# Kernel tuning notes

Measured on AMD Instinct MI355X. Metric: run time of the kernel, lower is better.

## Reference

```python
import jax, jax.numpy as jnp
import numpy as np
from jax import lax

H, W = 128, 128
K_JUNC = 300
STEPS = 32
THRESH = 0.008
BIAS_SPAN = 1
SCALE = 5.0
SENTINEL = K_JUNC * K_JUNC


def decode_hafm(angs, dist, bias):
    # angs [B,3,H,W], dist [B,1,H,W], bias [B,1,H,W] -> lines [B,3,H,W,4]
    bias_range = jnp.arange(-BIAS_SPAN, BIAS_SPAN + 1, dtype=jnp.float32).reshape(1, -1, 1, 1)
    d = jnp.clip(dist + bias * bias_range, 0.0, 1.0)  # [B,3,H,W]
    angle0 = (angs[:, 0:1] - 0.5) * jnp.pi * 2
    angle1 = angs[:, 1:2] * jnp.pi / 2
    angle2 = -angs[:, 2:3] * jnp.pi / 2
    c0, s0 = jnp.cos(angle0), jnp.sin(angle0)
    t1, t2 = jnp.tan(angle1), jnp.tan(angle2)
    x1 = (c0 - s0 * t1) * d * SCALE
    y1 = (s0 + c0 * t1) * d * SCALE
    x2 = (c0 - s0 * t2) * d * SCALE
    y2 = (s0 + c0 * t2) * d * SCALE
    y0, x0 = jnp.meshgrid(jnp.arange(H, dtype=jnp.float32), jnp.arange(W, dtype=jnp.float32), indexing='ij')
    x0 = x0[None, None]
    y0 = y0[None, None]
    x1 = jnp.clip(x1 + x0, 0, W - 1)
    y1 = jnp.clip(y1 + y0, 0, H - 1)
    x2 = jnp.clip(x2 + x0, 0, W - 1)
    y2 = jnp.clip(y2 + y0, 0, H - 1)
    return jnp.stack((x1, y1, x2, y2), axis=-1)


def propose_junctions(jloc, joff):
    # jloc [H,W], joff [2,H,W]; 3x3 NMS + top-K, thresholded junctions
    pooled = lax.reduce_window(jloc, -jnp.inf, lax.max, (3, 3), (1, 1), 'SAME')
    nms = jnp.where(jloc == pooled, jloc, 0.0)
    scores, idx = lax.top_k(nms.reshape(-1), K_JUNC)
    y = (idx // W).astype(jnp.float32)
    x = (idx % W).astype(jnp.float32)
    xs = x + joff[0].reshape(-1)[idx]
    ys = y + joff[1].reshape(-1)[idx]
    coords = jnp.stack([xs, ys], axis=-1)  # [K,2]
    valid = scores > THRESH
    coords = jnp.where(valid[:, None], coords, 1e6)
    return coords, scores


def bilinear_sample(fmap, px, py):
    # fmap [C,H,W]; px,py [N,S] -> [C,N,S]
    C = fmap.shape[0]
    px = jnp.clip(px, 0.0, W - 1)
    py = jnp.clip(py, 0.0, H - 1)
    x0 = jnp.floor(px)
    y0 = jnp.floor(py)
    x0i = x0.astype(jnp.int32)
    y0i = y0.astype(jnp.int32)
    x1i = jnp.minimum(x0i + 1, W - 1)
    y1i = jnp.minimum(y0i + 1, H - 1)
    wx = px - x0
    wy = py - y0
    flat = fmap.reshape(C, H * W)

    def g(yi, xi):
        return flat[:, (yi * W + xi).reshape(-1)].reshape(C, *px.shape)

    return (g(y0i, x0i) * (1 - wx) * (1 - wy)
            + g(y0i, x1i) * wx * (1 - wy)
            + g(y1i, x0i) * (1 - wx) * wy
            + g(y1i, x1i) * wx * wy)


def setup_inputs() -> dict:
    key = jax.random.key(0)
    ks = jax.random.split(key, 10)
    return {
        'features': jax.random.normal(ks[0], (1, 256, H, W), jnp.float32),
        'heatmaps': jax.random.normal(ks[1], (1, 9, H, W), jnp.float32),
        'fc1_w': jax.random.normal(ks[2], (128, 256), jnp.float32) * 0.05,
        'fc1_b': jax.random.normal(ks[3], (128,), jnp.float32) * 0.05,
        'w1': jax.random.normal(ks[4], (1024, 1024), jnp.float32) * 0.03,
        'b1': jnp.zeros((1024,), jnp.float32),
        'w2': jax.random.normal(ks[5], (1024, 1024), jnp.float32) * 0.03,
        'b2': jnp.zeros((1024,), jnp.float32),
        'w3': jax.random.normal(ks[6], (1, 1024), jnp.float32) * 0.03,
        'b3': jnp.zeros((1,), jnp.float32),
    }


def reference(features, heatmaps, fc1_w, fc1_b, w1, b1, w2, b2, w3, b3):
    angs = jax.nn.sigmoid(heatmaps[:, 0:3])
    dist = jax.nn.sigmoid(heatmaps[:, 3:4])
    bias = jax.nn.sigmoid(heatmaps[:, 4:5])
    jloc = jax.nn.softmax(heatmaps[:, 5:7], axis=1)[0, 1]  # [H,W]
    joff = jax.nn.sigmoid(heatmaps[0, 7:9])                # [2,H,W]

    junc, _ = propose_junctions(jloc, joff)                # [K,2]
    lines = decode_hafm(angs, dist, bias).reshape(-1, 4)   # [N,4], N=3*H*W
    N = lines.shape[0]

    # junction-to-endpoint matching (cdist + argmin)
    d1 = ((junc[:, None, :] - lines[None, :, :2]) ** 2).sum(-1)  # [K,N]
    d2 = ((junc[:, None, :] - lines[None, :, 2:]) ** 2).sum(-1)
    j1 = jnp.argmin(d1, axis=0)
    j2 = jnp.argmin(d2, axis=0)
    lo = jnp.minimum(j1, j2)
    hi = jnp.maximum(j1, j2)
    ids = jnp.where(lo < hi, lo * K_JUNC + hi, SENTINEL)
    # fixed-size dedup (masked analogue of torch unique(dim=0))
    uids = jnp.unique(ids, size=N, fill_value=SENTINEL)
    valid = uids < SENTINEL
    uids_safe = jnp.where(valid, uids, 0)
    p1 = junc[uids_safe // K_JUNC]
    p2 = junc[uids_safe % K_JUNC]
    line_coords = jnp.where(valid[:, None], jnp.concatenate([p1, p2], axis=-1), 0.0)  # [N,4]

    # LOI feature sampling
    loi = jnp.einsum('oc,chw->ohw', fc1_w, features[0]) + fc1_b[:, None, None]  # [128,H,W]
    t = jnp.linspace(0.0, 1.0, STEPS)[None, :]
    px = line_coords[:, 0:1] * t + line_coords[:, 2:3] * (1 - t)  # [N,32]
    py = line_coords[:, 1:2] * t + line_coords[:, 3:4] * (1 - t)
    feats = bilinear_sample(loi, px, py)            # [128,N,32]
    feats = feats.transpose(1, 0, 2)                # [N,128,32]
    feats = feats.reshape(N, 128, STEPS // 4, 4).max(-1)  # max_pool1d k=4
    feats = feats.reshape(N, 1024)

    h = jax.nn.relu(feats @ w1.T + b1)
    h = jax.nn.relu(h @ w2.T + b2)
    logits = (h @ w3.T + b3)[:, 0]
    line_scores = jax.nn.sigmoid(logits) * valid
    return line_coords, line_scores
```

## Files before the change

kernel.cpp:

```cpp
#include <hip/hip_runtime.h>
#include <math.h>

#define HH 128
#define WW 128
#define HW 16384
#define NLINES 49152
#define KJ 300
#define SENT 90000
#define THRESHV 0.008f
#define CAND_CAP 4096
#define BITWORDS 2816

typedef __attribute__((ext_vector_type(8))) short bf16x8;
typedef __attribute__((ext_vector_type(4))) float f32x4;

__device__ __forceinline__ float sigm(float x){ return 1.0f/(1.0f+expf(-x)); }

__device__ __forceinline__ short tobf(float f){
  unsigned u = __float_as_uint(f);
  unsigned r = u + 0x7FFFu + ((u >> 16) & 1u);
  return (short)(r >> 16);
}
__device__ __forceinline__ float bflo(unsigned u){ return __uint_as_float(u << 16); }
__device__ __forceinline__ float bfhi(unsigned u){ return __uint_as_float(u & 0xFFFF0000u); }

#define GLOAD_LDS16(g, l) \
  __builtin_amdgcn_global_load_lds((const __attribute__((address_space(1))) void*)(g), \
                                   (__attribute__((address_space(3))) void*)(l), 16, 0, 0)

__device__ __forceinline__ float jloc_at(const float* hm, int idx){
  float h5 = hm[5*HW + idx], h6 = hm[6*HW + idx];
  float mx = fmaxf(h5,h6);
  float e5 = expf(h5-mx), e6 = expf(h6-mx);
  return e6/(e5+e6);
}

__global__ __launch_bounds__(256) void k_front(const float* __restrict__ hm,
    const float* __restrict__ feat, const float* __restrict__ fc1w,
    float* __restrict__ lines, unsigned long long* __restrict__ cand,
    int* __restrict__ cand_count, short* __restrict__ featT, short* __restrict__ fc1b16){
  __shared__ float tile[32][33];
  int b = blockIdx.x, t = threadIdx.x;
  if (b < 64){
    int i = b*256 + t;
    float h0 = hm[i], h1 = hm[HW+i], h2 = hm[2*HW+i], h3 = hm[3*HW+i], h4 = hm[4*HW+i];
    float a0 = sigm(h0), a1 = sigm(h1), a2 = sigm(h2);
    float dist = sigm(h3), bias = sigm(h4);
    const float PI = 3.14159265358979323846f;
    float ang0 = (a0-0.5f)*(2.0f*PI);
    float c0 = cosf(ang0), s0 = sinf(ang0);
    float t1 = tanf(a1*(0.5f*PI));
    float t2 = tanf(-a2*(0.5f*PI));
    int y = i >> 7, x = i & 127;
    float fx = (float)x, fy = (float)y;
    #pragma unroll
    for (int c=0;c<3;c++){
      float d = fminf(fmaxf(dist + bias*(float)(c-1), 0.0f), 1.0f);
      float ds = d*5.0f;
      float x1 = fminf(fmaxf((c0 - s0*t1)*ds + fx, 0.0f), 127.0f);
      float y1 = fminf(fmaxf((s0 + c0*t1)*ds + fy, 0.0f), 127.0f);
      float x2 = fminf(fmaxf((c0 - s0*t2)*ds + fx, 0.0f), 127.0f);
      float y2 = fminf(fmaxf((s0 + c0*t2)*ds + fy, 0.0f), 127.0f);
      ((float4*)lines)[c*HW + i] = make_float4(x1,y1,x2,y2);
    }
    float v = jloc_at(hm, i);
    float m = v;
    for (int dy=-1; dy<=1; dy++){
      int ny = y + dy; if (ny < 0 || ny >= HH) continue;
      for (int dx=-1; dx<=1; dx++){
        int nx = x + dx; if (nx < 0 || nx >= WW) continue;
        m = fmaxf(m, jloc_at(hm, ny*WW + nx));
      }
    }
    if (v == m && v > THRESHV){
      int pos = atomicAdd(cand_count, 1);
      if (pos < CAND_CAP){
        unsigned int vb = __float_as_uint(v);
        cand[pos] = ((unsigned long long)vb << 32) | (unsigned long long)(0xFFFFFFFFu - (unsigned)i);
      }
    }
  } else if (b < 64 + 4096){
    int idx = b - 64;
    int p0 = (idx & 511) * 32, c0 = (idx >> 9) * 32;
    int tp = t & 31, tc = t >> 5;
    #pragma unroll
    for (int i=0; i<4; i++){
      int c = tc + i*8;
      tile[c][tp] = feat[(size_t)(c0 + c)*HW + p0 + tp];
    }
    __syncthreads();
    #pragma unroll
    for (int i=0; i<4; i++){
      int p = tc + i*8;
      featT[(size_t)(p0 + p)*256 + c0 + tp] = tobf(tile[tp][p]);
    }
  } else {
    int j = (b - 4160)*256 + t;
    fc1b16[j] = tobf(fc1w[j]);
  }
}

__global__ __launch_bounds__(1024) void k_mid(
    const unsigned long long* __restrict__ cand, const int* __restrict__ cand_count,
    const float* __restrict__ hm, float* __restrict__ junc,
    const short* __restrict__ featT, const short* __restrict__ fc1b16,
    const float* __restrict__ fc1b, short* __restrict__ loi,
    const float* __restrict__ w1, const float* __restrict__ w2,
    short* __restrict__ w1b, short* __restrict__ w2b){
  __shared__ __align__(16) char smem[CAND_CAP*8];
  int b = blockIdx.x, t = threadIdx.x;
  if (b == 0){
    unsigned long long* s = (unsigned long long*)smem;
    int count = *cand_count; if (count > CAND_CAP) count = CAND_CAP;
    int n2 = 512;
    while (n2 < count) n2 <<= 1;
    for (int i=t; i<n2; i+=1024) s[i] = (i < count) ? cand[i] : 0ull;
    __syncthreads();
    for (int k=2; k<=n2; k<<=1){
      for (int j=k>>1; j>0; j>>=1){
        for (int i=t; i<n2; i+=1024){
          int ixj = i ^ j;
          if (ixj > i){
            unsigned long long a = s[i], bb = s[ixj];
            bool desc = ((i & k) == 0);
            if (desc ? (a < bb) : (a > bb)){ s[i] = bb; s[ixj] = a; }
          }
        }
        __syncthreads();
      }
    }
    if (t < KJ){
      float jx = 1e6f, jy = 1e6f;
      if (t < count){
        unsigned idx = 0xFFFFFFFFu - (unsigned)(s[t] & 0xFFFFFFFFull);
        int yy = (int)(idx >> 7), xx = (int)(idx & 127u);
        jx = (float)xx + sigm(hm[7*HW + idx]);
        jy = (float)yy + sigm(hm[8*HW + idx]);
      }
      junc[2*t] = jx; junc[2*t+1] = jy;
    }
  } else if (b <= 256){
    if (t >= 256) return;
    short* As = (short*)smem;
    short* Bs = (short*)(smem + 8192);
    int rb = (b - 1) * 64;
    int lane = t & 63, wave = t >> 6;
    int l16 = lane & 15, quad = lane >> 4;
    int srow = lane >> 3, schunk = (lane & 7) ^ srow;
    f32x4 acc[8];
    #pragma unroll
    for (int g=0; g<8; g++) acc[g] = (f32x4){0,0,0,0};
    for (int k0=0; k0<256; k0+=64){
      #pragma unroll
      for (int i=0; i<2; i++){
        int r0 = wave*16 + i*8;
        GLOAD_LDS16(featT + (size_t)(rb + r0 + srow)*256 + k0 + schunk*8, &As[r0*64]);
      }
      #pragma unroll
      for (int i=0; i<4; i++){
        int r0 = wave*32 + i*8;
        GLOAD_LDS16(fc1b16 + (size_t)(r0 + srow)*256 + k0 + schunk*8, &Bs[r0*64]);
      }
      __syncthreads();
      #pragma unroll
      for (int s2=0; s2<2; s2++){
        int slot = (s2*4 + quad) ^ (l16 & 7);
        bf16x8 a = *(const bf16x8*)&As[(wave*16 + l16)*64 + slot*8];
        #pragma unroll
        for (int g=0; g<8; g++){
          bf16x8 bv = *(const bf16x8*)&Bs[(g*16 + l16)*64 + slot*8];
          acc[g] = __builtin_amdgcn_mfma_f32_16x16x32_bf16(a, bv, acc[g], 0, 0, 0);
        }
      }
      __syncthreads();
    }
    int rowbase = rb + wave*16 + quad*4;
    #pragma unroll
    for (int g=0; g<8; g++){
      int col = g*16 + l16;
      float bs = fc1b[col];
      #pragma unroll
      for (int r=0; r<4; r++)
        loi[(size_t)(rowbase + r)*128 + col] = tobf(acc[g][r] + bs);
    }
  } else {
    int j = (b - 257)*1024 + t;
    w1b[j] = tobf(w1[j]);
    w2b[j] = tobf(w2[j]);
  }
}

__global__ void k_match(const float* __restrict__ lines, const float* __restrict__ junc,
                        int* __restrict__ ids){
  __shared__ float jx[KJ], jy[KJ];
  int t = threadIdx.x;
  for (int k=t; k<KJ; k+=blockDim.x){ jx[k] = junc[2*k]; jy[k] = junc[2*k+1]; }
  __syncthreads();
  int n = blockIdx.x*blockDim.x + t;
  if (n >= NLINES) return;
  float4 L = ((const float4*)lines)[n];
  float b1 = 1e30f, b2 = 1e30f; int j1 = 0, j2 = 0;
  #pragma unroll 4
  for (int k=0; k<KJ; k++){
    float dx1 = jx[k]-L.x, dy1 = jy[k]-L.y;
    float d1 = dx1*dx1 + dy1*dy1;
    float dx2 = jx[k]-L.z, dy2 = jy[k]-L.w;
    float d2 = dx2*dx2 + dy2*dy2;
    if (d1 < b1){ b1 = d1; j1 = k; }
    if (d2 < b2){ b2 = d2; j2 = k; }
  }
  int lo = min(j1,j2), hi = max(j1,j2);
  ids[n] = (lo < hi) ? (lo*KJ + hi) : SENT;
}

__global__ __launch_bounds__(1024) void k_unique(const int* __restrict__ ids,
    int* __restrict__ uid_list, int* __restrict__ mcount){
  __shared__ unsigned bm[BITWORDS];
  __shared__ int wsum[16];
  int t = threadIdx.x;
  for (int i=t; i<BITWORDS; i+=1024) bm[i] = 0u;
  __syncthreads();
  for (int n=t; n<NLINES; n+=1024){
    int id = ids[n];
    if (id < SENT) atomicOr(&bm[id>>5], 1u << (id & 31));
  }
  __syncthreads();
  int w0 = t*3;
  int local = 0;
  for (int w=w0; w<w0+3; w++) if (w < BITWORDS) local += __popc(bm[w]);
  int v = local;
  #pragma unroll
  for (int d=1; d<64; d<<=1){
    int nv = __shfl_up(v, d, 64);
    if ((t & 63) >= d) v += nv;
  }
  if ((t & 63) == 63) wsum[t >> 6] = v;
  __syncthreads();
  if (t < 16){
    int x = wsum[t];
    #pragma unroll
    for (int d=1; d<16; d<<=1){
      int nv = __shfl_up(x, d, 16);
      if (t >= d) x += nv;
    }
    wsum[t] = x;
  }
  __syncthreads();
  int base = v - local + ((t >> 6) ? wsum[(t >> 6) - 1] : 0);
  for (int w=w0; w<w0+3; w++){
    if (w >= BITWORDS) break;
    unsigned bits = bm[w];
    while (bits){
      int bb = __ffs(bits) - 1;
      uid_list[base++] = w*32 + bb;
      bits &= bits - 1;
    }
  }
  if (t == 1023) *mcount = base;
}

__global__ void k_coords(const int* __restrict__ uid_list, const int* __restrict__ mcount,
                         const float* __restrict__ junc, float* __restrict__ out){
  int r = blockIdx.x*blockDim.x + threadIdx.x;
  if (r >= NLINES) return;
  int M = *mcount;
  float4 v = make_float4(0.f,0.f,0.f,0.f);
  if (r < M){
    int id = uid_list[r];
    int lo = id / KJ, hi = id % KJ;
    v = make_float4(junc[2*lo], junc[2*lo+1], junc[2*hi], junc[2*hi+1]);
  } else {
    out[4*NLINES + r] = 0.0f;
  }
  ((float4*)out)[r] = v;
}

__global__ __launch_bounds__(256) void k_sample(const float* __restrict__ out,
    const short* __restrict__ loi, const int* __restrict__ mcount,
    short* __restrict__ fbuf, float* __restrict__ logit, int* __restrict__ cnt,
    int ncnt, int chunk0, int chunk){
  __shared__ int4   sOffs[32];
  __shared__ float4 sWts[32];
  int M = *mcount;
  int t = threadIdx.x;
  if (t == 0 && blockIdx.x < ncnt) cnt[blockIdx.x] = 0;
  int q  = t >> 6;
  int c2 = (t & 63) << 1;
  for (int l = blockIdx.x; l < chunk && chunk0 + l < M; l += gridDim.x){
    int r = chunk0 + l;
    if (t == 0) logit[l] = 0.0f;
    __syncthreads();
    if (t < 32){
      float4 C = ((const float4*)out)[r];
      float tt = (float)t * (1.0f/31.0f);
      float px = C.x*tt + C.z*(1.0f-tt);
      float py = C.y*tt + C.w*(1.0f-tt);
      px = fminf(fmaxf(px, 0.0f), 127.0f);
      py = fminf(fmaxf(py, 0.0f), 127.0f);
      float x0 = floorf(px), y0 = floorf(py);
      int x0i = (int)x0, y0i = (int)y0;
      int x1i = min(x0i+1, 127), y1i = min(y0i+1, 127);
      float wx = px - x0, wy = py - y0;
      sOffs[t] = make_int4((y0i*WW + x0i)*128, (y0i*WW + x1i)*128,
                           (y1i*WW + x0i)*128, (y1i*WW + x1i)*128);
      sWts[t]  = make_float4((1.0f-wx)*(1.0f-wy), wx*(1.0f-wy),
                             (1.0f-wx)*wy,        wx*wy);
    }
    __syncthreads();
    float gl0=-1e30f, gl1=-1e30f, gh0=-1e30f, gh1=-1e30f;
    #pragma unroll
    for (int j=0; j<8; j++){
      int s = q*8 + j;
      int4 o   = sOffs[s];
      float4 w = sWts[s];
      unsigned u00 = *(const unsigned*)&loi[o.x + c2];
      unsigned u01 = *(const unsigned*)&loi[o.y + c2];
      unsigned u10 = *(const unsigned*)&loi[o.z + c2];
      unsigned u11 = *(const unsigned*)&loi[o.w + c2];
      float vlo = w.x*bflo(u00) + w.y*bflo(u01) + w.z*bflo(u10) + w.w*bflo(u11);
      float vhi = w.x*bfhi(u00) + w.y*bfhi(u01) + w.z*bfhi(u10) + w.w*bfhi(u11);
      if (j < 4){ gl0 = fmaxf(gl0, vlo); gh0 = fmaxf(gh0, vhi); }
      else      { gl1 = fmaxf(gl1, vlo); gh1 = fmaxf(gh1, vhi); }
    }
    unsigned plo = ((unsigned)(unsigned short)tobf(gl0)) | (((unsigned)(unsigned short)tobf(gl1)) << 16);
    unsigned phi = ((unsigned)(unsigned short)tobf(gh0)) | (((unsigned)(unsigned short)tobf(gh1)) << 16);
    *(unsigned*)&fbuf[(size_t)l*1024 + c2*8 + q*2]     = plo;
    *(unsigned*)&fbuf[(size_t)l*1024 + (c2+1)*8 + q*2] = phi;
  }
}

template<int MODE>
__global__ __launch_bounds__(256) void k_mlp(const short* __restrict__ A,
    const short* __restrict__ B, const float* __restrict__ bias,
    short* __restrict__ Hout, const float* __restrict__ w3,
    const float* __restrict__ b3, float* __restrict__ logit,
    int* __restrict__ cnt, const int* __restrict__ mcount,
    int chunk0, float* __restrict__ outScore){
  int M = *mcount;
  int rb = blockIdx.x * 128;
  if (chunk0 + rb >= M) return;
  int cb = blockIdx.y * 128;
  __shared__ short As[128*64];
  __shared__ short Bs[128*64];
  __shared__ int sflag;
  int lane = threadIdx.x & 63, wave = threadIdx.x >> 6;
  int l16 = lane & 15, quad = lane >> 4;
  int srow = lane >> 3, schunk = (lane & 7) ^ srow;
  f32x4 acc0[8], acc1[8];
  #pragma unroll
  for (int g=0; g<8; g++){ acc0[g] = (f32x4){0,0,0,0}; acc1[g] = (f32x4){0,0,0,0}; }
  for (int k0=0; k0<1024; k0+=64){
    #pragma unroll
    for (int i=0; i<4; i++){
      int r0 = wave*32 + i*8;
      GLOAD_LDS16(A + (size_t)(rb + r0 + srow)*1024 + k0 + schunk*8, &As[r0*64]);
      GLOAD_LDS16(B + (size_t)(cb + r0 + srow)*1024 + k0 + schunk*8, &Bs[r0*64]);
    }
    __syncthreads();
    #pragma unroll
    for (int s=0; s<2; s++){
      int slot = (s*4 + quad) ^ (l16 & 7);
      bf16x8 a0 = *(const bf16x8*)&As[(wave*32 + l16)*64 + slot*8];
      bf16x8 a1 = *(const bf16x8*)&As[(wave*32 + 16 + l16)*64 + slot*8];
      #pragma unroll
      for (int g=0; g<8; g++){
        bf16x8 bv = *(const bf16x8*)&Bs[(g*16 + l16)*64 + slot*8];
        acc0[g] = __builtin_amdgcn_mfma_f32_16x16x32_bf16(a0, bv, acc0[g], 0, 0, 0);
        acc1[g] = __builtin_amdgcn_mfma_f32_16x16x32_bf16(a1, bv, acc1[g], 0, 0, 0);
      }
    }
    __syncthreads();
  }
  int r0b = rb + wave*32 + quad*4;
  int r1b = r0b + 16;
  if (MODE == 0){
    #pragma unroll
    for (int g=0; g<8; g++){
      int col = cb + g*16 + l16;
      float bs = bias[col];
      #pragma unroll
      for (int r=0; r<4; r++){
        Hout[(size_t)(r0b + r)*1024 + col] = tobf(fmaxf(acc0[g][r] + bs, 0.0f));
        Hout[(size_t)(r1b + r)*1024 + col] = tobf(fmaxf(acc1[g][r] + bs, 0.0f));
      }
    }
  } else {
    float p0[4] = {0,0,0,0}, p1[4] = {0,0,0,0};
    #pragma unroll
    for (int g=0; g<8; g++){
      int col = cb + g*16 + l16;
      float bs = bias[col], wv = w3[col];
      #pragma unroll
      for (int r=0; r<4; r++){
        p0[r] += fmaxf(acc0[g][r] + bs, 0.0f) * wv;
        p1[r] += fmaxf(acc1[g][r] + bs, 0.0f) * wv;
      }
    }
    #pragma unroll
    for (int r=0; r<4; r++){
      #pragma unroll
      for (int m=1; m<16; m<<=1){
        p0[r] += __shfl_xor(p0[r], m, 16);
        p1[r] += __shfl_xor(p1[r], m, 16);
      }
    }
    if (l16 == 0){
      #pragma unroll
      for (int r=0; r<4; r++){
        atomicAdd(&logit[r0b + r], p0[r]);
        atomicAdd(&logit[r1b + r], p1[r]);
      }
    }
    __syncthreads();
    if (threadIdx.x == 0){
      __threadfence();
      int old = atomicAdd(&cnt[blockIdx.x], 1);
      sflag = (old == 7) ? 1 : 0;
    }
    __syncthreads();
    if (sflag){
      __threadfence();
      if (threadIdx.x < 128){
        int row = rb + threadIdx.x;
        int rg = chunk0 + row;
        if (rg < M){
          float lg = atomicAdd(&logit[row], 0.0f) + b3[0];
          outScore[4*NLINES + rg] = 1.0f/(1.0f + expf(-lg));
        }
      }
    }
  }
}

extern "C" void kernel_launch(void* const* d_in, const int* in_sizes, int n_in,
                              void* d_out, int out_size, void* d_ws, size_t ws_size,
                              hipStream_t stream){
  const float* features = (const float*)d_in[0];
  const float* heatmaps = (const float*)d_in[1];
  const float* fc1_w    = (const float*)d_in[2];
  const float* fc1_b    = (const float*)d_in[3];
  const float* w1       = (const float*)d_in[4];
  const float* b1       = (const float*)d_in[5];
  const float* w2       = (const float*)d_in[6];
  const float* b2       = (const float*)d_in[7];
  const float* w3       = (const float*)d_in[8];
  const float* b3       = (const float*)d_in[9];
  float* out = (float*)d_out;

  char* ws = (char*)d_ws;
  size_t off = 0;
  auto alloc = [&](size_t bytes) -> void* {
    void* p = ws + off;
    off = (off + bytes + 255) & ~(size_t)255;
    return p;
  };
  float* lines     = (float*)alloc((size_t)NLINES*16);
  unsigned long long* cand = (unsigned long long*)alloc(CAND_CAP*8);
  int*   cand_count= (int*)alloc(4);
  float* junc      = (float*)alloc(KJ*2*4);
  int*   ids       = (int*)alloc((size_t)NLINES*4);
  int*   uid_list  = (int*)alloc((size_t)NLINES*4);
  int*   mcount    = (int*)alloc(4);
  int*   cnt       = (int*)alloc((NLINES/128)*4);
  short* loi       = (short*)alloc((size_t)HW*128*2);
  short* featT     = (short*)alloc((size_t)HW*256*2);
  short* fc1b16    = (short*)alloc((size_t)128*256*2);
  short* w1b       = (short*)alloc((size_t)1024*1024*2);
  short* w2b       = (short*)alloc((size_t)1024*1024*2);
  size_t fixed = off;

  const int chunk_opts[7] = {49152, 24576, 12288, 8192, 4096, 2048, 1024};
  int CHUNK = 1024;
  for (int ci=0; ci<7; ci++){
    size_t need = fixed + (size_t)chunk_opts[ci]*1024*2*2 + (size_t)chunk_opts[ci]*4 + 1024;
    if (need <= ws_size){ CHUNK = chunk_opts[ci]; break; }
  }
  short* fbuf  = (short*)alloc((size_t)CHUNK*1024*2);
  short* h1buf = (short*)alloc((size_t)CHUNK*1024*2);
  float* logit = (float*)alloc((size_t)CHUNK*4);

  hipMemsetAsync(cand_count, 0, 4, stream);
  k_front<<<4288, 256, 0, stream>>>(heatmaps, features, fc1_w, lines, cand,
                                    cand_count, featT, fc1b16);
  k_mid  <<<1281, 1024, 0, stream>>>(cand, cand_count, heatmaps, junc, featT,
                                     fc1b16, fc1_b, loi, w1, w2, w1b, w2b);
  k_match<<<NLINES/256, 256, 0, stream>>>(lines, junc, ids);
  k_unique<<<1, 1024, 0, stream>>>(ids, uid_list, mcount);
  k_coords<<<NLINES/256, 256, 0, stream>>>(uid_list, mcount, junc, out);

  int nchunk = NLINES / CHUNK;
  for (int ci=0; ci<nchunk; ci++){
    int chunk0 = ci * CHUNK;
    k_sample<<<2048, 256, 0, stream>>>(out, loi, mcount, fbuf, logit, cnt,
                                       CHUNK/128, chunk0, CHUNK);
    dim3 g1(CHUNK/128, 8);
    k_mlp<0><<<g1, 256, 0, stream>>>(fbuf, w1b, b1, h1buf, nullptr, nullptr,
                                     nullptr, nullptr, mcount, chunk0, nullptr);
    k_mlp<2><<<g1, 256, 0, stream>>>(h1buf, w2b, b2, nullptr, w3, b3,
                                     logit, cnt, mcount, chunk0, out);
  }
}
```

Measured before the change: 224.1 us.

## Fuse match, unique and coords kernels with a last-block bitmap compaction

Junction matching now sets bits directly in a global bitmap with atomics. The last block to finish, found through an atomic completion counter, compacts the bitmap into the unique id list. This removes the single-block k_unique pass over all ids, the ids buffer and the k_coords launch; line coordinates are now written inside k_sample. The weight bf16 conversion moves from k_mid into the match kernel, and the feature transpose uses float4 loads and ushort4 stores. The cost is global atomics plus a serialized 256-thread compaction tail in the final block.

```diff
diff --git a/kernel.cpp b/kernel.cpp
--- a/kernel.cpp
+++ b/kernel.cpp
@@ -82,18 +82,19 @@
   } else if (b < 64 + 4096){
     int idx = b - 64;
     int p0 = (idx & 511) * 32, c0 = (idx >> 9) * 32;
-    int tp = t & 31, tc = t >> 5;
-    #pragma unroll
-    for (int i=0; i<4; i++){
-      int c = tc + i*8;
-      tile[c][tp] = feat[(size_t)(c0 + c)*HW + p0 + tp];
-    }
-    __syncthreads();
-    #pragma unroll
-    for (int i=0; i<4; i++){
-      int p = tc + i*8;
-      featT[(size_t)(p0 + p)*256 + c0 + tp] = tobf(tile[tp][p]);
-    }
+    int c  = t >> 3;
+    int p4 = (t & 7) * 4;
+    float4 v = *(const float4*)&feat[(size_t)(c0 + c)*HW + p0 + p4];
+    tile[c][p4+0] = v.x; tile[c][p4+1] = v.y; tile[c][p4+2] = v.z; tile[c][p4+3] = v.w;
+    __syncthreads();
+    int p  = t >> 3;
+    int cg = (t & 7) * 4;
+    ushort4 o;
+    o.x = (unsigned short)tobf(tile[cg+0][p]);
+    o.y = (unsigned short)tobf(tile[cg+1][p]);
+    o.z = (unsigned short)tobf(tile[cg+2][p]);
+    o.w = (unsigned short)tobf(tile[cg+3][p]);
+    *(ushort4*)&featT[(size_t)(p0 + p)*256 + c0 + cg] = o;
   } else {
     int j = (b - 4160)*256 + t;
     fc1b16[j] = tobf(fc1w[j]);
@@ -104,9 +105,7 @@
     const unsigned long long* __restrict__ cand, const int* __restrict__ cand_count,
     const float* __restrict__ hm, float* __restrict__ junc,
     const short* __restrict__ featT, const short* __restrict__ fc1b16,
-    const float* __restrict__ fc1b, short* __restrict__ loi,
-    const float* __restrict__ w1, const float* __restrict__ w2,
-    short* __restrict__ w1b, short* __restrict__ w2b){
+    const float* __restrict__ fc1b, short* __restrict__ loi){
   __shared__ __align__(16) char smem[CAND_CAP*8];
   int b = blockIdx.x, t = threadIdx.x;
   if (b == 0){
@@ -139,7 +138,7 @@
       }
       junc[2*t] = jx; junc[2*t+1] = jy;
     }
-  } else if (b <= 256){
+  } else {
     if (t >= 256) return;
     short* As = (short*)smem;
     short* Bs = (short*)(smem + 8192);
@@ -183,51 +182,58 @@
       for (int r=0; r<4; r++)
         loi[(size_t)(rowbase + r)*128 + col] = tobf(acc[g][r] + bs);
     }
+  }
+}
+
+__global__ __launch_bounds__(256) void k_match(const float* __restrict__ lines,
+    const float* __restrict__ junc, unsigned* __restrict__ bm, int* __restrict__ mdone,
+    int* __restrict__ uid_list, int* __restrict__ mcount,
+    const float* __restrict__ w1, const float* __restrict__ w2,
+    short* __restrict__ w1b, short* __restrict__ w2b){
+  __shared__ float jx[KJ], jy[KJ];
+  __shared__ int wsum[4];
+  __shared__ int lastflag;
+  int b = blockIdx.x, t = threadIdx.x;
+  if (b < 192){
+    for (int k=t; k<KJ; k+=256){ jx[k] = junc[2*k]; jy[k] = junc[2*k+1]; }
+    __syncthreads();
+    int n = b*256 + t;
+    float4 L = ((const float4*)lines)[n];
+    float b1 = 1e30f, b2 = 1e30f; int j1 = 0, j2 = 0;
+    #pragma unroll 4
+    for (int k=0; k<KJ; k++){
+      float dx1 = jx[k]-L.x, dy1 = jy[k]-L.y;
+      float d1 = dx1*dx1 + dy1*dy1;
+      float dx2 = jx[k]-L.z, dy2 = jy[k]-L.w;
+      float d2 = dx2*dx2 + dy2*dy2;
+      if (d1 < b1){ b1 = d1; j1 = k; }
+      if (d2 < b2){ b2 = d2; j2 = k; }
+    }
+    int lo = min(j1,j2), hi = max(j1,j2);
+    if (lo < hi){
+      int id = lo*KJ + hi;
+      atomicOr(&bm[id >> 5], 1u << (id & 31));
+    }
   } else {
-    int j = (b - 257)*1024 + t;
+    int j = (b - 192)*256 + t;
     w1b[j] = tobf(w1[j]);
     w2b[j] = tobf(w2[j]);
   }
-}
-
-__global__ void k_match(const float* __restrict__ lines, const float* __restrict__ junc,
-                        int* __restrict__ ids){
-  __shared__ float jx[KJ], jy[KJ];
-  int t = threadIdx.x;
-  for (int k=t; k<KJ; k+=blockDim.x){ jx[k] = junc[2*k]; jy[k] = junc[2*k+1]; }
   __syncthreads();
-  int n = blockIdx.x*blockDim.x + t;
-  if (n >= NLINES) return;
-  float4 L = ((const float4*)lines)[n];
-  float b1 = 1e30f, b2 = 1e30f; int j1 = 0, j2 = 0;
-  #pragma unroll 4
-  for (int k=0; k<KJ; k++){
-    float dx1 = jx[k]-L.x, dy1 = jy[k]-L.y;
-    float d1 = dx1*dx1 + dy1*dy1;
-    float dx2 = jx[k]-L.z, dy2 = jy[k]-L.w;
-    float d2 = dx2*dx2 + dy2*dy2;
-    if (d1 < b1){ b1 = d1; j1 = k; }
-    if (d2 < b2){ b2 = d2; j2 = k; }
-  }
-  int lo = min(j1,j2), hi = max(j1,j2);
-  ids[n] = (lo < hi) ? (lo*KJ + hi) : SENT;
-}
-
-__global__ __launch_bounds__(1024) void k_unique(const int* __restrict__ ids,
-    int* __restrict__ uid_list, int* __restrict__ mcount){
-  __shared__ unsigned bm[BITWORDS];
-  __shared__ int wsum[16];
-  int t = threadIdx.x;
-  for (int i=t; i<BITWORDS; i+=1024) bm[i] = 0u;
+  __threadfence();
+  if (t == 0){
+    int old = atomicAdd(mdone, 1);
+    lastflag = (old == (int)gridDim.x - 1) ? 1 : 0;
+  }
   __syncthreads();
-  for (int n=t; n<NLINES; n+=1024){
-    int id = ids[n];
-    if (id < SENT) atomicOr(&bm[id>>5], 1u << (id & 31));
-  }
-  __syncthreads();
-  int w0 = t*3;
+  if (!lastflag) return;
+  unsigned w[11];
   int local = 0;
-  for (int w=w0; w<w0+3; w++) if (w < BITWORDS) local += __popc(bm[w]);
+  #pragma unroll
+  for (int i=0; i<11; i++){
+    w[i] = atomicOr(&bm[t*11 + i], 0u);
+    local += __popc(w[i]);
+  }
   int v = local;
   #pragma unroll
   for (int d=1; d<64; d<<=1){
@@ -236,46 +242,31 @@
   }
   if ((t & 63) == 63) wsum[t >> 6] = v;
   __syncthreads();
-  if (t < 16){
+  if (t < 4){
     int x = wsum[t];
     #pragma unroll
-    for (int d=1; d<16; d<<=1){
-      int nv = __shfl_up(x, d, 16);
+    for (int d=1; d<4; d<<=1){
+      int nv = __shfl_up(x, d, 4);
       if (t >= d) x += nv;
     }
     wsum[t] = x;
   }
   __syncthreads();
   int base = v - local + ((t >> 6) ? wsum[(t >> 6) - 1] : 0);
-  for (int w=w0; w<w0+3; w++){
-    if (w >= BITWORDS) break;
-    unsigned bits = bm[w];
+  #pragma unroll
+  for (int i=0; i<11; i++){
+    unsigned bits = w[i];
     while (bits){
       int bb = __ffs(bits) - 1;
-      uid_list[base++] = w*32 + bb;
+      uid_list[base++] = (t*11 + i)*32 + bb;
       bits &= bits - 1;
     }
   }
-  if (t == 1023) *mcount = base;
-}
-
-__global__ void k_coords(const int* __restrict__ uid_list, const int* __restrict__ mcount,
-                         const float* __restrict__ junc, float* __restrict__ out){
-  int r = blockIdx.x*blockDim.x + threadIdx.x;
-  if (r >= NLINES) return;
-  int M = *mcount;
-  float4 v = make_float4(0.f,0.f,0.f,0.f);
-  if (r < M){
-    int id = uid_list[r];
-    int lo = id / KJ, hi = id % KJ;
-    v = make_float4(junc[2*lo], junc[2*lo+1], junc[2*hi], junc[2*hi+1]);
-  } else {
-    out[4*NLINES + r] = 0.0f;
-  }
-  ((float4*)out)[r] = v;
-}
-
-__global__ __launch_bounds__(256) void k_sample(const float* __restrict__ out,
+  if (t == 255) *mcount = wsum[3];
+}
+
+__global__ __launch_bounds__(256) void k_sample(float* __restrict__ out,
+    const int* __restrict__ uid_list, const float* __restrict__ junc,
     const short* __restrict__ loi, const int* __restrict__ mcount,
     short* __restrict__ fbuf, float* __restrict__ logit, int* __restrict__ cnt,
     int ncnt, int chunk0, int chunk){
@@ -286,46 +277,57 @@
   if (t == 0 && blockIdx.x < ncnt) cnt[blockIdx.x] = 0;
   int q  = t >> 6;
   int c2 = (t & 63) << 1;
-  for (int l = blockIdx.x; l < chunk && chunk0 + l < M; l += gridDim.x){
+  for (int l = blockIdx.x; l < chunk; l += gridDim.x){
     int r = chunk0 + l;
-    if (t == 0) logit[l] = 0.0f;
-    __syncthreads();
-    if (t < 32){
-      float4 C = ((const float4*)out)[r];
-      float tt = (float)t * (1.0f/31.0f);
-      float px = C.x*tt + C.z*(1.0f-tt);
-      float py = C.y*tt + C.w*(1.0f-tt);
-      px = fminf(fmaxf(px, 0.0f), 127.0f);
-      py = fminf(fmaxf(py, 0.0f), 127.0f);
-      float x0 = floorf(px), y0 = floorf(py);
-      int x0i = (int)x0, y0i = (int)y0;
-      int x1i = min(x0i+1, 127), y1i = min(y0i+1, 127);
-      float wx = px - x0, wy = py - y0;
-      sOffs[t] = make_int4((y0i*WW + x0i)*128, (y0i*WW + x1i)*128,
-                           (y1i*WW + x0i)*128, (y1i*WW + x1i)*128);
-      sWts[t]  = make_float4((1.0f-wx)*(1.0f-wy), wx*(1.0f-wy),
-                             (1.0f-wx)*wy,        wx*wy);
-    }
-    __syncthreads();
-    float gl0=-1e30f, gl1=-1e30f, gh0=-1e30f, gh1=-1e30f;
-    #pragma unroll
-    for (int j=0; j<8; j++){
-      int s = q*8 + j;
-      int4 o   = sOffs[s];
-      float4 w = sWts[s];
-      unsigned u00 = *(const unsigned*)&loi[o.x + c2];
-      unsigned u01 = *(const unsigned*)&loi[o.y + c2];
-      unsigned u10 = *(const unsigned*)&loi[o.z + c2];
-      unsigned u11 = *(const unsigned*)&loi[o.w + c2];
-      float vlo = w.x*bflo(u00) + w.y*bflo(u01) + w.z*bflo(u10) + w.w*bflo(u11);
-      float vhi = w.x*bfhi(u00) + w.y*bfhi(u01) + w.z*bfhi(u10) + w.w*bfhi(u11);
-      if (j < 4){ gl0 = fmaxf(gl0, vlo); gh0 = fmaxf(gh0, vhi); }
-      else      { gl1 = fmaxf(gl1, vlo); gh1 = fmaxf(gh1, vhi); }
-    }
-    unsigned plo = ((unsigned)(unsigned short)tobf(gl0)) | (((unsigned)(unsigned short)tobf(gl1)) << 16);
-    unsigned phi = ((unsigned)(unsigned short)tobf(gh0)) | (((unsigned)(unsigned short)tobf(gh1)) << 16);
-    *(unsigned*)&fbuf[(size_t)l*1024 + c2*8 + q*2]     = plo;
-    *(unsigned*)&fbuf[(size_t)l*1024 + (c2+1)*8 + q*2] = phi;
+    if (r < M){
+      if (t == 0) logit[l] = 0.0f;
+      __syncthreads();
+      if (t < 32){
+        int id = uid_list[r];
+        int lo = id / KJ, hi = id % KJ;
+        float2 P1 = ((const float2*)junc)[lo];
+        float2 P2 = ((const float2*)junc)[hi];
+        if (t == 0) ((float4*)out)[r] = make_float4(P1.x, P1.y, P2.x, P2.y);
+        float tt = (float)t * (1.0f/31.0f);
+        float px = P1.x*tt + P2.x*(1.0f-tt);
+        float py = P1.y*tt + P2.y*(1.0f-tt);
+        px = fminf(fmaxf(px, 0.0f), 127.0f);
+        py = fminf(fmaxf(py, 0.0f), 127.0f);
+        float x0 = floorf(px), y0 = floorf(py);
+        int x0i = (int)x0, y0i = (int)y0;
+        int x1i = min(x0i+1, 127), y1i = min(y0i+1, 127);
+        float wx = px - x0, wy = py - y0;
+        sOffs[t] = make_int4((y0i*WW + x0i)*128, (y0i*WW + x1i)*128,
+                             (y1i*WW + x0i)*128, (y1i*WW + x1i)*128);
+        sWts[t]  = make_float4((1.0f-wx)*(1.0f-wy), wx*(1.0f-wy),
+                               (1.0f-wx)*wy,        wx*wy);
+      }
+      __syncthreads();
+      float gl0=-1e30f, gl1=-1e30f, gh0=-1e30f, gh1=-1e30f;
+      #pragma unroll
+      for (int j=0; j<8; j++){
+        int s = q*8 + j;
+        int4 o   = sOffs[s];
+        float4 w = sWts[s];
+        unsigned u00 = *(const unsigned*)&loi[o.x + c2];
+        unsigned u01 = *(const unsigned*)&loi[o.y + c2];
+        unsigned u10 = *(const unsigned*)&loi[o.z + c2];
+        unsigned u11 = *(const unsigned*)&loi[o.w + c2];
+        float vlo = w.x*bflo(u00) + w.y*bflo(u01) + w.z*bflo(u10) + w.w*bflo(u11);
+        float vhi = w.x*bfhi(u00) + w.y*bfhi(u01) + w.z*bfhi(u10) + w.w*bfhi(u11);
+        if (j < 4){ gl0 = fmaxf(gl0, vlo); gh0 = fmaxf(gh0, vhi); }
+        else      { gl1 = fmaxf(gl1, vlo); gh1 = fmaxf(gh1, vhi); }
+      }
+      unsigned plo = ((unsigned)(unsigned short)tobf(gl0)) | (((unsigned)(unsigned short)tobf(gl1)) << 16);
+      unsigned phi = ((unsigned)(unsigned short)tobf(gh0)) | (((unsigned)(unsigned short)tobf(gh1)) << 16);
+      *(unsigned*)&fbuf[(size_t)l*1024 + c2*8 + q*2]     = plo;
+      *(unsigned*)&fbuf[(size_t)l*1024 + (c2+1)*8 + q*2] = phi;
+    } else {
+      if (t == 0){
+        ((float4*)out)[r] = make_float4(0.f,0.f,0.f,0.f);
+        out[4*NLINES + r] = 0.0f;
+      }
+    }
   }
 }
 
@@ -456,9 +458,11 @@
   };
   float* lines     = (float*)alloc((size_t)NLINES*16);
   unsigned long long* cand = (unsigned long long*)alloc(CAND_CAP*8);
-  int*   cand_count= (int*)alloc(4);
+  int*      cand_count = (int*)alloc(4);
+  int*      mdone      = (int*)alloc(4);
+  unsigned* bitmap     = (unsigned*)alloc(BITWORDS*4);
+  size_t zlen = (size_t)((char*)(bitmap + BITWORDS) - (char*)cand_count);
   float* junc      = (float*)alloc(KJ*2*4);
-  int*   ids       = (int*)alloc((size_t)NLINES*4);
   int*   uid_list  = (int*)alloc((size_t)NLINES*4);
   int*   mcount    = (int*)alloc(4);
   int*   cnt       = (int*)alloc((NLINES/128)*4);
@@ -479,20 +483,19 @@
   short* h1buf = (short*)alloc((size_t)CHUNK*1024*2);
   float* logit = (float*)alloc((size_t)CHUNK*4);
 
-  hipMemsetAsync(cand_count, 0, 4, stream);
+  hipMemsetAsync(cand_count, 0, zlen, stream);
   k_front<<<4288, 256, 0, stream>>>(heatmaps, features, fc1_w, lines, cand,
                                     cand_count, featT, fc1b16);
-  k_mid  <<<1281, 1024, 0, stream>>>(cand, cand_count, heatmaps, junc, featT,
-                                     fc1b16, fc1_b, loi, w1, w2, w1b, w2b);
-  k_match<<<NLINES/256, 256, 0, stream>>>(lines, junc, ids);
-  k_unique<<<1, 1024, 0, stream>>>(ids, uid_list, mcount);
-  k_coords<<<NLINES/256, 256, 0, stream>>>(uid_list, mcount, junc, out);
+  k_mid  <<<257, 1024, 0, stream>>>(cand, cand_count, heatmaps, junc, featT,
+                                    fc1b16, fc1_b, loi);
+  k_match<<<4288, 256, 0, stream>>>(lines, junc, bitmap, mdone, uid_list, mcount,
+                                    w1, w2, w1b, w2b);
 
   int nchunk = NLINES / CHUNK;
   for (int ci=0; ci<nchunk; ci++){
     int chunk0 = ci * CHUNK;
-    k_sample<<<2048, 256, 0, stream>>>(out, loi, mcount, fbuf, logit, cnt,
-                                       CHUNK/128, chunk0, CHUNK);
+    k_sample<<<2048, 256, 0, stream>>>(out, uid_list, junc, loi, mcount, fbuf,
+                                       logit, cnt, CHUNK/128, chunk0, CHUNK);
     dim3 g1(CHUNK/128, 8);
     k_mlp<0><<<g1, 256, 0, stream>>>(fbuf, w1b, b1, h1buf, nullptr, nullptr,
                                      nullptr, nullptr, mcount, chunk0, nullptr);
```

Result: slower. 472.6 us (+110.8%).
